# Kernel optimization log

Measured on AMD Instinct MI355X. Metric: run time of the kernel, lower is better.

## Reference

```python
import jax, jax.numpy as jnp
import numpy as np

N_NODES = 50000
N_EDGES = 800000
F_IN = 11
HID = 128
N_ACT = 6


def _gcn_conv(x, W, b, src, dst, n):
    # PyG GCNConv: x' = D^{-1/2}(A+I)D^{-1/2} (x W) + b, with self-loops.
    h = x @ W  # [N, H]
    ones = jnp.ones(src.shape[0], dtype=h.dtype)
    deg = jax.ops.segment_sum(ones, dst, num_segments=n) + 1.0  # +1 self-loop
    dinv = jax.lax.rsqrt(deg)
    enorm = dinv[src] * dinv[dst]  # [E]
    msg = h[src] * enorm[:, None]  # gather + scale
    agg = jax.ops.segment_sum(msg, dst, num_segments=n)
    agg = agg + h * (dinv * dinv)[:, None]  # self-loop contribution (norm = 1/deg)
    return agg + b


def _mlp2(x, W1, b1, W2, b2):
    return jax.nn.relu(x @ W1 + b1) @ W2 + b2


def setup_inputs() -> dict:
    key = jax.random.key(0)
    ks = jax.random.split(key, 16)
    def g(k, shape, scale):
        return jax.random.normal(k, shape, dtype=jnp.float32) * scale
    x = g(ks[0], (N_NODES, F_IN), 1.0)
    edge_index = jax.random.randint(ks[1], (2, N_EDGES), 0, N_NODES, dtype=jnp.int64)
    return {
        "x": x,
        "edge_index": edge_index,
        "W1": g(ks[2], (F_IN, HID), 1.0 / np.sqrt(F_IN)),
        "b1": jnp.zeros((HID,), jnp.float32),
        "W2": g(ks[3], (HID, HID), 1.0 / np.sqrt(HID)),
        "b2": jnp.zeros((HID,), jnp.float32),
        "W3": g(ks[4], (HID, HID), 1.0 / np.sqrt(HID)),
        "b3": jnp.zeros((HID,), jnp.float32),
        "Wv1": g(ks[5], (HID, HID), 1.0 / np.sqrt(HID)),
        "bv1": jnp.zeros((HID,), jnp.float32),
        "Wv2": g(ks[6], (HID, 1), 1.0 / np.sqrt(HID)),
        "bv2": jnp.zeros((1,), jnp.float32),
        "Wa1": g(ks[7], (HID, HID), 1.0 / np.sqrt(HID)),
        "ba1": jnp.zeros((HID,), jnp.float32),
        "Wa2": g(ks[8], (HID, N_ACT), 1.0 / np.sqrt(HID)),
        "ba2": jnp.zeros((N_ACT,), jnp.float32),
    }


def reference(x, edge_index, W1, b1, W2, b2, W3, b3,
              Wv1, bv1, Wv2, bv2, Wa1, ba1, Wa2, ba2):
    src, dst = edge_index[0], edge_index[1]
    n = x.shape[0]
    h = jax.nn.relu(_gcn_conv(x, W1, b1, src, dst, n))
    h = jax.nn.relu(_gcn_conv(h, W2, b2, src, dst, n))
    h = jax.nn.relu(_gcn_conv(h, W3, b3, src, dst, n))
    # global_mean_pool with batch = zeros -> single-graph mean over nodes
    g = jnp.mean(h, axis=0, keepdims=True)  # [1, HID]
    value = _mlp2(g, Wv1, bv1, Wv2, bv2)          # [1, 1]
    advantage = _mlp2(g, Wa1, ba1, Wa2, ba2)      # [1, N_ACT]
    q = value + (advantage - jnp.mean(advantage, axis=-1, keepdims=True))
    return q
```

## Files before the change

kernel.cpp:

```cpp
#include <hip/hip_runtime.h>

#define HID 128
#define F_IN 11
#define FP 16
#define N_ACT 6
#define EPB 2048
#define LMAX 6144
#define CAP 8192

typedef __bf16 bf16;
typedef __bf16 v8bf __attribute__((ext_vector_type(8)));
typedef float f32x4 __attribute__((ext_vector_type(4)));
typedef float v2f __attribute__((ext_vector_type(2)));

__device__ inline float lo16(unsigned u) { return __uint_as_float(u << 16); }
__device__ inline float hi16(unsigned u) { return __uint_as_float(u & 0xffff0000u); }
__device__ inline unsigned pk2(float a, float b) {
  union { bf16 h; unsigned short u; } x, y;
  x.h = (bf16)a; y.h = (bf16)b;
  return ((unsigned)y.u << 16) | x.u;
}
__device__ inline v2f fp8_dec_lo(unsigned v) {
  return __builtin_amdgcn_cvt_pk_f32_fp8(v, false);
}
__device__ inline v2f fp8_dec_hi(unsigned v) {
  return __builtin_amdgcn_cvt_pk_f32_fp8(v, true);
}
__device__ inline unsigned fp8_enc2_lo(float a, float b, unsigned old) {
  return __builtin_amdgcn_cvt_pk_fp8_f32(a, b, old, false);
}
__device__ inline unsigned fp8_enc2_hi(float a, float b, unsigned old) {
  return __builtin_amdgcn_cvt_pk_fp8_f32(a, b, old, true);
}
__device__ inline unsigned char fp8_enc1(float v) {
  return (unsigned char)(__builtin_amdgcn_cvt_pk_fp8_f32(v, v, 0u, false) & 0xffu);
}


__global__ __launch_bounds__(256) void k_init(int* __restrict__ gcur,
                                              float* __restrict__ gsum, int nbkt) {
  int t = threadIdx.x;
  if (t < nbkt) gcur[t] = t * CAP;
  if (t < HID) gsum[t] = 0.f;
}

__global__ __launch_bounds__(256) void k_part(const int* __restrict__ esrc,
                                              const int* __restrict__ edst,
                                              int* __restrict__ gcur,
                                              unsigned* __restrict__ ebuf,
                                              const float* __restrict__ W2,
                                              const float* __restrict__ W3,
                                              bf16* __restrict__ WT2,
                                              bf16* __restrict__ WT3,
                                              int E, int nbkt) {
  __shared__ int hist[256], lofs[256], lcur[256], gbase[256];
  __shared__ unsigned sbuf[EPB];
  int t = threadIdx.x;
  hist[t] = 0;
  if (blockIdx.x < 64) {
    int i = blockIdx.x * 256 + t;
    int nn = i >> 7, k = i & 127;
    WT2[i] = (bf16)W2[k * 128 + nn];
    WT3[i] = (bf16)W3[k * 128 + nn];
  }
  __syncthreads();
  int start = blockIdx.x * EPB, end = min(E, start + EPB);
  unsigned u[8];
#pragma unroll
  for (int i = 0; i < 8; ++i) {
    int e = start + t + i * 256;
    if (e < end) {
      int s = esrc[e], d = edst[e];
      u[i] = ((unsigned)d << 16) | (unsigned)s;
      atomicAdd(&hist[d >> 8], 1);
    }
  }
  __syncthreads();
  int h = hist[t];
  lofs[t] = h;
  __syncthreads();
  for (int off = 1; off < 256; off <<= 1) {
    int x = (t >= off) ? lofs[t - off] : 0;
    __syncthreads();
    lofs[t] += x;
    __syncthreads();
  }
  lcur[t] = lofs[t] - h;
  if (t < nbkt && h) gbase[t] = atomicAdd(&gcur[t], h);
  __syncthreads();
#pragma unroll
  for (int i = 0; i < 8; ++i) {
    int e = start + t + i * 256;
    if (e < end) {
      int b = (int)(u[i] >> 24);
      int p = atomicAdd(&lcur[b], 1);
      sbuf[p] = u[i];
    }
  }
  __syncthreads();
  int m = end - start;
  for (int i = t; i < m; i += 256) {
    unsigned v = sbuf[i];
    int b = (int)(v >> 24);
    int excl = lofs[b] - hist[b];
    ebuf[gbase[b] + (i - excl)] = v;
  }
}

__global__ __launch_bounds__(1024) void k_local(const unsigned* __restrict__ ebuf,
                                                const int* __restrict__ gcur,
                                                int2* __restrict__ rbe,
                                                float* __restrict__ dinv,
                                                unsigned short* __restrict__ cs,
                                                const float* __restrict__ x,
                                                bf16* __restrict__ xs, int n) {
  __shared__ int hist[256], lofs[256], cur[256];
  __shared__ float dsh[256];
  __shared__ unsigned sb[LMAX];
  int b = blockIdx.x, t = threadIdx.x;
  int rb = b * CAP, re = gcur[b];
  int m = re - rb;
  int nbase = b << 8;
  bool fit = (m <= LMAX);
  if (t < 256) hist[t] = 0;
  __syncthreads();
  if (fit) {
    for (int i = t; i < m; i += 1024) {
      unsigned u = ebuf[rb + i];
      sb[i] = u;
      atomicAdd(&hist[(int)(u >> 16) - nbase], 1);
    }
  } else {
    for (int i = t; i < m; i += 1024)
      atomicAdd(&hist[(int)(ebuf[rb + i] >> 16) - nbase], 1);
  }
  __syncthreads();
  int h = 0;
  if (t < 256) { h = hist[t]; lofs[t] = h; }
  __syncthreads();
  for (int off = 1; off < 256; off <<= 1) {
    int v = (t < 256 && t >= off) ? lofs[t - off] : 0;
    __syncthreads();
    if (t < 256) lofs[t] += v;
    __syncthreads();
  }
  if (t < 256) {
    int excl = lofs[t] - h;
    cur[t] = rb + excl;
    float dv = rsqrtf((float)h + 1.0f);
    dsh[t] = dv;
    int g = nbase + t;
    if (g < n) {
      rbe[g] = make_int2(rb + excl, rb + lofs[t]);
      dinv[g] = dv;
    }
  }
  __syncthreads();
  if (fit) {
    for (int i = t; i < m; i += 1024) {
      unsigned u = sb[i];
      int p = atomicAdd(&cur[(int)(u >> 16) - nbase], 1);
      cs[p] = (unsigned short)(u & 0xffffu);
    }
  } else {
    for (int i = t; i < m; i += 1024) {
      unsigned u = ebuf[rb + i];
      int p = atomicAdd(&cur[(int)(u >> 16) - nbase], 1);
      cs[p] = (unsigned short)(u & 0xffffu);
    }
  }
  for (int i = t; i < 256 * FP; i += 1024) {
    int node = nbase + (i >> 4), c = i & 15;
    if (node < n)
      xs[(size_t)node * FP + c] =
          (bf16)((c < F_IN) ? x[(size_t)node * F_IN + c] * dsh[i >> 4] : 0.f);
  }
}


__global__ __launch_bounds__(256) void k_layer1(const bf16* __restrict__ xs,
                                                const float* __restrict__ dinv,
                                                const int2* __restrict__ rbe,
                                                const unsigned short* __restrict__ cs,
                                                const float* __restrict__ W1,
                                                const float* __restrict__ b1,
                                                unsigned* __restrict__ H8, int n) {
  __shared__ float Ws[F_IN * HID];
  __shared__ float A1s[64][17];
  int tid = threadIdx.x;
  int n0 = blockIdx.x * 64;
  for (int i = tid; i < F_IN * HID; i += 256) Ws[i] = W1[i];
  int wave = tid >> 6, lane = tid & 63;
  int g8 = lane >> 3, c = lane & 7;
  const unsigned* xs2 = (const unsigned*)xs;
#pragma unroll
  for (int r = 0; r < 2; ++r) {
    int row = wave * 16 + r * 8 + g8;
    int node = n0 + row;
    unsigned sv = 0;
    int j = 0, jend = 0;
    float dd = 0.f;
    if (node < n) {
      sv = xs2[(size_t)node * 8 + c];
      int2 be = rbe[node];
      j = be.x; jend = be.y;
      dd = dinv[node];
    }
    float ax = lo16(sv), ay = hi16(sv);
    for (; j < jend; j += 4) {
#pragma unroll
      for (int k = 0; k < 4; ++k) {
        int jj = j + k;
        bool ok = jj < jend;
        int sidx = cs[ok ? jj : jend - 1];
        unsigned v = xs2[(size_t)sidx * 8 + c];
        float mm = ok ? 1.f : 0.f;
        ax = fmaf(lo16(v), mm, ax);
        ay = fmaf(hi16(v), mm, ay);
      }
    }
    A1s[row][c * 2] = ax * dd;
    A1s[row][c * 2 + 1] = ay * dd;
  }
  __syncthreads();
  int tc = tid & 15, tr = tid >> 4;
  float bb[8];
#pragma unroll
  for (int j = 0; j < 8; ++j) bb[j] = b1[tc * 8 + j];
#pragma unroll
  for (int i = 0; i < 4; ++i) {
    int row = tr * 4 + i;
    int node = n0 + row;
    if (node >= n) continue;
    float acc[8];
#pragma unroll
    for (int j = 0; j < 8; ++j) acc[j] = 0.f;
#pragma unroll
    for (int k = 0; k < F_IN; ++k) {
      float xk = A1s[row][k];
      const float* wr = &Ws[k * HID + tc * 8];
#pragma unroll
      for (int j = 0; j < 8; ++j) acc[j] = fmaf(xk, wr[j], acc[j]);
    }
    float dd = dinv[node];
    float o[8];
#pragma unroll
    for (int j = 0; j < 8; ++j) o[j] = fmaxf(acc[j] + bb[j], 0.f) * dd;
    unsigned w0 = 0, w1 = 0;
    w0 = fp8_enc2_lo(o[0], o[1], w0);
    w0 = fp8_enc2_hi(o[2], o[3], w0);
    w1 = fp8_enc2_lo(o[4], o[5], w1);
    w1 = fp8_enc2_hi(o[6], o[7], w1);
    ((uint2*)H8)[(size_t)node * 16 + tc] = make_uint2(w0, w1);
  }
}


template <bool FINAL>
__global__ __launch_bounds__(512) void k_layer(const unsigned* __restrict__ tab,
                                               const float* __restrict__ dinv,
                                               const int2* __restrict__ rbe,
                                               const unsigned short* __restrict__ cs,
                                               const bf16* __restrict__ WT,
                                               const float* __restrict__ b,
                                               unsigned char* __restrict__ H8,
                                               float* __restrict__ gsum, int n) {
  __shared__ bf16 Asm[64 * 128];
  __shared__ float colacc[128];
  int tid = threadIdx.x;
  int n0 = blockIdx.x * 64;
  if (FINAL && tid < 128) colacc[tid] = 0.f;
  int wave = tid >> 6, lane = tid & 63;
  int sub = lane >> 5;
  int c = lane & 31;
#pragma unroll
  for (int r = 0; r < 4; ++r) {
    int row = wave * 8 + r * 2 + sub;
    int node = n0 + row;
    float a0 = 0.f, a1 = 0.f, a2 = 0.f, a3 = 0.f, dd = 0.f;
    int j = 0, jend = 0;
    if (node < n) {
      unsigned sv = tab[(size_t)node * 32 + c];
      v2f lo = fp8_dec_lo(sv), hi = fp8_dec_hi(sv);
      a0 = lo.x; a1 = lo.y; a2 = hi.x; a3 = hi.y;
      int2 be = rbe[node];
      j = be.x; jend = be.y;
      dd = dinv[node];
    }
    for (; j < jend; j += 8) {
#pragma unroll
      for (int k = 0; k < 8; ++k) {
        int jj = j + k;
        bool ok = jj < jend;
        int sidx = cs[ok ? jj : jend - 1];
        unsigned v = tab[(size_t)sidx * 32 + c];
        float mm = ok ? 1.f : 0.f;
        v2f lo = fp8_dec_lo(v), hi = fp8_dec_hi(v);
        a0 = fmaf(lo.x, mm, a0);
        a1 = fmaf(lo.y, mm, a1);
        a2 = fmaf(hi.x, mm, a2);
        a3 = fmaf(hi.y, mm, a3);
      }
    }
    int kc = c >> 1, half = c & 1;
    uint2 w = make_uint2(pk2(a0 * dd, a1 * dd), pk2(a2 * dd, a3 * dd));
    *(uint2*)((char*)Asm + row * 256 + ((kc ^ (row & 7)) << 4) + (half << 3)) = w;
  }
  __syncthreads();
  int l15 = lane & 15, g = lane >> 4;
  int rg = (wave & 3) * 16;
  int cg = (wave >> 2) * 64;
  f32x4 acc[4];
#pragma unroll
  for (int f = 0; f < 4; ++f) acc[f] = (f32x4){0.f, 0.f, 0.f, 0.f};
  int arow = rg + l15;
#pragma unroll
  for (int kk = 0; kk < 4; ++kk) {
    int kc = kk * 4 + g;
    v8bf a = *(const v8bf*)((const char*)Asm + arow * 256 + ((kc ^ (arow & 7)) << 4));
#pragma unroll
    for (int f = 0; f < 4; ++f) {
      int nrow = cg + f * 16 + l15;
      v8bf bfr = *(const v8bf*)(WT + (size_t)nrow * 128 + kc * 8);
      acc[f] = __builtin_amdgcn_mfma_f32_16x16x32_bf16(a, bfr, acc[f], 0, 0, 0);
    }
  }
  int nodebase = n0 + rg + g * 4;
  if (FINAL) {
#pragma unroll
    for (int f = 0; f < 4; ++f) {
      int col = cg + f * 16 + l15;
      float bias = b[col];
      float sf = 0.f;
#pragma unroll
      for (int j = 0; j < 4; ++j) {
        int node = nodebase + j;
        if (node < n) sf += fmaxf(acc[f][j] + bias, 0.f);
      }
      atomicAdd(&colacc[col], sf);
    }
    __syncthreads();
    if (tid < 128) atomicAdd(&gsum[tid], colacc[tid]);
  } else {
    float dv[4];
#pragma unroll
    for (int j = 0; j < 4; ++j)
      dv[j] = (nodebase + j < n) ? dinv[nodebase + j] : 1.f;
#pragma unroll
    for (int f = 0; f < 4; ++f) {
      int col = cg + f * 16 + l15;
      float bias = b[col];
#pragma unroll
      for (int j = 0; j < 4; ++j) {
        int node = nodebase + j;
        if (node < n) {
          float v = fmaxf(acc[f][j] + bias, 0.f) * dv[j];
          H8[(size_t)node * 128 + col] = fp8_enc1(v);
        }
      }
    }
  }
}


__global__ __launch_bounds__(128) void k_head(const float* __restrict__ gsum,
    const float* __restrict__ Wv1, const float* __restrict__ bv1,
    const float* __restrict__ Wv2, const float* __restrict__ bv2,
    const float* __restrict__ Wa1, const float* __restrict__ ba1,
    const float* __restrict__ Wa2, const float* __restrict__ ba2,
    float* __restrict__ out, int n) {
  __shared__ float gs[HID], ha[HID], red[2], advs[N_ACT], vsh;
  int t = threadIdx.x;
  gs[t] = gsum[t] * (1.0f / (float)n);
  __syncthreads();
  float av = bv1[t], aa = ba1[t];
  for (int k = 0; k < HID; ++k) {
    float gk = gs[k];
    av = fmaf(gk, Wv1[k * HID + t], av);
    aa = fmaf(gk, Wa1[k * HID + t], aa);
  }
  float hv = fmaxf(av, 0.f);
  ha[t] = fmaxf(aa, 0.f);
  float pv = hv * Wv2[t];
#pragma unroll
  for (int o = 32; o > 0; o >>= 1) pv += __shfl_down(pv, o);
  if ((t & 63) == 0) red[t >> 6] = pv;
  __syncthreads();
  if (t == 0) vsh = red[0] + red[1] + bv2[0];
  if (t < N_ACT) {
    float adv = ba2[t];
    for (int j = 0; j < HID; ++j) adv = fmaf(ha[j], Wa2[j * N_ACT + t], adv);
    advs[t] = adv;
  }
  __syncthreads();
  if (t < N_ACT) {
    float m = 0.f;
#pragma unroll
    for (int a = 0; a < N_ACT; ++a) m += advs[a];
    m *= (1.0f / N_ACT);
    out[t] = vsh + advs[t] - m;
  }
}


extern "C" void kernel_launch(void* const* d_in, const int* in_sizes, int n_in,
                              void* d_out, int out_size, void* d_ws, size_t ws_size,
                              hipStream_t stream) {
  const float* x   = (const float*)d_in[0];
  const int*   ei  = (const int*)d_in[1];
  const float* W1  = (const float*)d_in[2];
  const float* b1  = (const float*)d_in[3];
  const float* W2  = (const float*)d_in[4];
  const float* b2  = (const float*)d_in[5];
  const float* W3  = (const float*)d_in[6];
  const float* b3  = (const float*)d_in[7];
  const float* Wv1 = (const float*)d_in[8];
  const float* bv1 = (const float*)d_in[9];
  const float* Wv2 = (const float*)d_in[10];
  const float* bv2 = (const float*)d_in[11];
  const float* Wa1 = (const float*)d_in[12];
  const float* ba1 = (const float*)d_in[13];
  const float* Wa2 = (const float*)d_in[14];
  const float* ba2 = (const float*)d_in[15];
  float* out = (float*)d_out;

  const int N = in_sizes[0] / F_IN;
  const int E = in_sizes[1] / 2;
  const int* esrc = ei;
  const int* edst = ei + E;
  const int nbkt = (N + 255) >> 8;
  const int gE = (E + EPB - 1) / EPB;

  char* p = (char*)d_ws;
  auto alloc = [&](size_t bytes) {
    void* r = (void*)p;
    p += (bytes + 1023) & ~(size_t)1023;
    return r;
  };
  unsigned* ebuf   = (unsigned*)alloc((size_t)nbkt * CAP * 4);
  int*   gcur      = (int*)alloc((size_t)nbkt * 4);
  int2*  rbe       = (int2*)alloc((size_t)N * 8);
  float* dinv      = (float*)alloc((size_t)N * 4);
  unsigned short* cs = (unsigned short*)alloc((size_t)nbkt * CAP * 2);
  bf16*  xs        = (bf16*)alloc((size_t)N * FP * 2);
  bf16*  WT2       = (bf16*)alloc(128 * 128 * 2);
  bf16*  WT3       = (bf16*)alloc(128 * 128 * 2);
  unsigned* H8a    = (unsigned*)alloc((size_t)N * 128);
  unsigned* H8b    = (unsigned*)alloc((size_t)N * 128);
  float* gsum      = (float*)alloc(HID * 4);

  k_init<<<1, 256, 0, stream>>>(gcur, gsum, nbkt);
  k_part<<<gE, 256, 0, stream>>>(esrc, edst, gcur, ebuf, W2, W3, WT2, WT3, E, nbkt);
  k_local<<<nbkt, 1024, 0, stream>>>(ebuf, gcur, rbe, dinv, cs, x, xs, N);

  k_layer1<<<(N + 63) / 64, 256, 0, stream>>>(xs, dinv, rbe, cs, W1, b1, H8a, N);

  int gL = (N + 63) / 64;
  k_layer<false><<<gL, 512, 0, stream>>>(H8a, dinv, rbe, cs, WT2, b2,
                                         (unsigned char*)H8b, gsum, N);
  k_layer<true><<<gL, 512, 0, stream>>>(H8b, dinv, rbe, cs, WT3, b3,
                                        (unsigned char*)nullptr, gsum, N);

  k_head<<<1, 128, 0, stream>>>(gsum, Wv1, bv1, Wv2, bv2, Wa1, ba1, Wa2, ba2, out, N);
}
```

Baseline: 146.9 us.

## Pad CSR neighbor lists to multiples of 16 with zero-row sentinel, unmask gathers

Each node's neighbor segment in the CSR index array is padded up to a multiple of 16. The padding entries point to a sentinel node n whose feature rows (xs, H8a, H8b) are zeroed in k_init. This removes the per-edge bounds masking from the gather loops. The k_layer gather now loads 16 indices at once with two aligned uint4 loads, issues 16 independent feature loads, and halves the node tile per block from 64 to 32 to launch more blocks. The cost is extra gathers of the cached zero row and more CSR capacity use per bucket, which could overflow CAP on skewed graphs.

```diff
diff --git a/kernel.cpp b/kernel.cpp
--- a/kernel.cpp
+++ b/kernel.cpp
@@ -38,11 +38,17 @@
 
 
 __global__ __launch_bounds__(256) void k_init(int* __restrict__ gcur,
-                                              float* __restrict__ gsum, int nbkt) {
+                                              float* __restrict__ gsum,
+                                              unsigned* __restrict__ xsN,
+                                              unsigned* __restrict__ H8aN,
+                                              unsigned* __restrict__ H8bN, int nbkt) {
   int t = threadIdx.x;
   if (t < nbkt) gcur[t] = t * CAP;
   if (t < HID) gsum[t] = 0.f;
-}
+  if (t < 8) xsN[t] = 0u;
+  if (t < 32) { H8aN[t] = 0u; H8bN[t] = 0u; }
+}
+
 
 __global__ __launch_bounds__(256) void k_part(const int* __restrict__ esrc,
                                               const int* __restrict__ edst,
@@ -114,7 +120,7 @@
                                                 unsigned short* __restrict__ cs,
                                                 const float* __restrict__ x,
                                                 bf16* __restrict__ xs, int n) {
-  __shared__ int hist[256], lofs[256], cur[256];
+  __shared__ int hist[256], lofs[256], cur[256], realh[256];
   __shared__ float dsh[256];
   __shared__ unsigned sb[LMAX];
   int b = blockIdx.x, t = threadIdx.x;
@@ -135,8 +141,13 @@
       atomicAdd(&hist[(int)(ebuf[rb + i] >> 16) - nbase], 1);
   }
   __syncthreads();
-  int h = 0;
-  if (t < 256) { h = hist[t]; lofs[t] = h; }
+  int h = 0, hp = 0;
+  if (t < 256) {
+    h = hist[t];
+    realh[t] = h;
+    hp = (h + 15) & ~15;
+    lofs[t] = hp;
+  }
   __syncthreads();
   for (int off = 1; off < 256; off <<= 1) {
     int v = (t < 256 && t >= off) ? lofs[t - off] : 0;
@@ -145,13 +156,13 @@
     __syncthreads();
   }
   if (t < 256) {
-    int excl = lofs[t] - h;
-    cur[t] = rb + excl;
+    int pexcl = lofs[t] - hp;
+    cur[t] = rb + pexcl;
     float dv = rsqrtf((float)h + 1.0f);
     dsh[t] = dv;
     int g = nbase + t;
     if (g < n) {
-      rbe[g] = make_int2(rb + excl, rb + lofs[t]);
+      rbe[g] = make_int2(rb + pexcl, rb + pexcl + hp);
       dinv[g] = dv;
     }
   }
@@ -168,6 +179,13 @@
       int p = atomicAdd(&cur[(int)(u >> 16) - nbase], 1);
       cs[p] = (unsigned short)(u & 0xffffu);
     }
+  }
+  __syncthreads();
+  if (t < 256) {
+    int hh = realh[t];
+    int hpp = (hh + 15) & ~15;
+    int base = cur[t];
+    for (int i = hh; i < hpp; ++i) cs[base + (i - hh)] = (unsigned short)n;
   }
   for (int i = t; i < 256 * FP; i += 1024) {
     int node = nbase + (i >> 4), c = i & 15;
@@ -210,13 +228,9 @@
     for (; j < jend; j += 4) {
 #pragma unroll
       for (int k = 0; k < 4; ++k) {
-        int jj = j + k;
-        bool ok = jj < jend;
-        int sidx = cs[ok ? jj : jend - 1];
-        unsigned v = xs2[(size_t)sidx * 8 + c];
-        float mm = ok ? 1.f : 0.f;
-        ax = fmaf(lo16(v), mm, ax);
-        ay = fmaf(hi16(v), mm, ay);
+        unsigned v = xs2[(size_t)cs[j + k] * 8 + c];
+        ax += lo16(v);
+        ay += hi16(v);
       }
     }
     A1s[row][c * 2] = ax * dd;
@@ -265,62 +279,70 @@
                                                const float* __restrict__ b,
                                                unsigned char* __restrict__ H8,
                                                float* __restrict__ gsum, int n) {
-  __shared__ bf16 Asm[64 * 128];
+  __shared__ bf16 Asm[32 * 128];
   __shared__ float colacc[128];
   int tid = threadIdx.x;
-  int n0 = blockIdx.x * 64;
+  int n0 = blockIdx.x * 32;
   if (FINAL && tid < 128) colacc[tid] = 0.f;
   int wave = tid >> 6, lane = tid & 63;
   int sub = lane >> 5;
   int c = lane & 31;
 #pragma unroll
-  for (int r = 0; r < 4; ++r) {
-    int row = wave * 8 + r * 2 + sub;
+  for (int r = 0; r < 2; ++r) {
+    int row = wave * 4 + r * 2 + sub;
     int node = n0 + row;
-    float a0 = 0.f, a1 = 0.f, a2 = 0.f, a3 = 0.f, dd = 0.f;
+    v2f acc01 = (v2f){0.f, 0.f}, acc23 = (v2f){0.f, 0.f};
+    float dd = 0.f;
     int j = 0, jend = 0;
     if (node < n) {
       unsigned sv = tab[(size_t)node * 32 + c];
-      v2f lo = fp8_dec_lo(sv), hi = fp8_dec_hi(sv);
-      a0 = lo.x; a1 = lo.y; a2 = hi.x; a3 = hi.y;
+      acc01 = fp8_dec_lo(sv);
+      acc23 = fp8_dec_hi(sv);
       int2 be = rbe[node];
       j = be.x; jend = be.y;
       dd = dinv[node];
     }
-    for (; j < jend; j += 8) {
-#pragma unroll
-      for (int k = 0; k < 8; ++k) {
-        int jj = j + k;
-        bool ok = jj < jend;
-        int sidx = cs[ok ? jj : jend - 1];
-        unsigned v = tab[(size_t)sidx * 32 + c];
-        float mm = ok ? 1.f : 0.f;
-        v2f lo = fp8_dec_lo(v), hi = fp8_dec_hi(v);
-        a0 = fmaf(lo.x, mm, a0);
-        a1 = fmaf(lo.y, mm, a1);
-        a2 = fmaf(hi.x, mm, a2);
-        a3 = fmaf(hi.y, mm, a3);
+    for (; j < jend; j += 16) {
+      uint4 cv0 = *(const uint4*)(cs + j);
+      uint4 cv1 = *(const uint4*)(cs + j + 8);
+      unsigned sx[16];
+      sx[0] = cv0.x & 0xffffu;  sx[1] = cv0.x >> 16;
+      sx[2] = cv0.y & 0xffffu;  sx[3] = cv0.y >> 16;
+      sx[4] = cv0.z & 0xffffu;  sx[5] = cv0.z >> 16;
+      sx[6] = cv0.w & 0xffffu;  sx[7] = cv0.w >> 16;
+      sx[8] = cv1.x & 0xffffu;  sx[9] = cv1.x >> 16;
+      sx[10] = cv1.y & 0xffffu; sx[11] = cv1.y >> 16;
+      sx[12] = cv1.z & 0xffffu; sx[13] = cv1.z >> 16;
+      sx[14] = cv1.w & 0xffffu; sx[15] = cv1.w >> 16;
+      unsigned vv[16];
+#pragma unroll
+      for (int k = 0; k < 16; ++k) vv[k] = tab[(size_t)sx[k] * 32 + c];
+#pragma unroll
+      for (int k = 0; k < 16; ++k) {
+        acc01 += fp8_dec_lo(vv[k]);
+        acc23 += fp8_dec_hi(vv[k]);
       }
     }
     int kc = c >> 1, half = c & 1;
-    uint2 w = make_uint2(pk2(a0 * dd, a1 * dd), pk2(a2 * dd, a3 * dd));
+    uint2 w = make_uint2(pk2(acc01.x * dd, acc01.y * dd),
+                         pk2(acc23.x * dd, acc23.y * dd));
     *(uint2*)((char*)Asm + row * 256 + ((kc ^ (row & 7)) << 4) + (half << 3)) = w;
   }
   __syncthreads();
   int l15 = lane & 15, g = lane >> 4;
-  int rg = (wave & 3) * 16;
-  int cg = (wave >> 2) * 64;
-  f32x4 acc[4];
-#pragma unroll
-  for (int f = 0; f < 4; ++f) acc[f] = (f32x4){0.f, 0.f, 0.f, 0.f};
+  int rg = (wave & 1) * 16;
+  int cbase = (wave >> 1) * 32;
+  f32x4 acc[2];
+#pragma unroll
+  for (int f = 0; f < 2; ++f) acc[f] = (f32x4){0.f, 0.f, 0.f, 0.f};
   int arow = rg + l15;
 #pragma unroll
   for (int kk = 0; kk < 4; ++kk) {
     int kc = kk * 4 + g;
     v8bf a = *(const v8bf*)((const char*)Asm + arow * 256 + ((kc ^ (arow & 7)) << 4));
 #pragma unroll
-    for (int f = 0; f < 4; ++f) {
-      int nrow = cg + f * 16 + l15;
+    for (int f = 0; f < 2; ++f) {
+      int nrow = cbase + f * 16 + l15;
       v8bf bfr = *(const v8bf*)(WT + (size_t)nrow * 128 + kc * 8);
       acc[f] = __builtin_amdgcn_mfma_f32_16x16x32_bf16(a, bfr, acc[f], 0, 0, 0);
     }
@@ -328,8 +350,8 @@
   int nodebase = n0 + rg + g * 4;
   if (FINAL) {
 #pragma unroll
-    for (int f = 0; f < 4; ++f) {
-      int col = cg + f * 16 + l15;
+    for (int f = 0; f < 2; ++f) {
+      int col = cbase + f * 16 + l15;
       float bias = b[col];
       float sf = 0.f;
 #pragma unroll
@@ -347,8 +369,8 @@
     for (int j = 0; j < 4; ++j)
       dv[j] = (nodebase + j < n) ? dinv[nodebase + j] : 1.f;
 #pragma unroll
-    for (int f = 0; f < 4; ++f) {
-      int col = cg + f * 16 + l15;
+    for (int f = 0; f < 2; ++f) {
+      int col = cbase + f * 16 + l15;
       float bias = b[col];
 #pragma unroll
       for (int j = 0; j < 4; ++j) {
@@ -442,20 +464,21 @@
   int2*  rbe       = (int2*)alloc((size_t)N * 8);
   float* dinv      = (float*)alloc((size_t)N * 4);
   unsigned short* cs = (unsigned short*)alloc((size_t)nbkt * CAP * 2);
-  bf16*  xs        = (bf16*)alloc((size_t)N * FP * 2);
+  bf16*  xs        = (bf16*)alloc((size_t)(N + 1) * FP * 2);
   bf16*  WT2       = (bf16*)alloc(128 * 128 * 2);
   bf16*  WT3       = (bf16*)alloc(128 * 128 * 2);
-  unsigned* H8a    = (unsigned*)alloc((size_t)N * 128);
-  unsigned* H8b    = (unsigned*)alloc((size_t)N * 128);
+  unsigned* H8a    = (unsigned*)alloc((size_t)(N + 1) * 128);
+  unsigned* H8b    = (unsigned*)alloc((size_t)(N + 1) * 128);
   float* gsum      = (float*)alloc(HID * 4);
 
-  k_init<<<1, 256, 0, stream>>>(gcur, gsum, nbkt);
+  k_init<<<1, 256, 0, stream>>>(gcur, gsum, (unsigned*)(xs + (size_t)N * FP),
+                                H8a + (size_t)N * 32, H8b + (size_t)N * 32, nbkt);
   k_part<<<gE, 256, 0, stream>>>(esrc, edst, gcur, ebuf, W2, W3, WT2, WT3, E, nbkt);
   k_local<<<nbkt, 1024, 0, stream>>>(ebuf, gcur, rbe, dinv, cs, x, xs, N);
 
   k_layer1<<<(N + 63) / 64, 256, 0, stream>>>(xs, dinv, rbe, cs, W1, b1, H8a, N);
 
-  int gL = (N + 63) / 64;
+  int gL = (N + 31) / 32;
   k_layer<false><<<gL, 512, 0, stream>>>(H8a, dinv, rbe, cs, WT2, b2,
                                          (unsigned char*)H8b, gsum, N);
   k_layer<true><<<gL, 512, 0, stream>>>(H8b, dinv, rbe, cs, WT3, b3,
```

Result: no change. 145.9 us (median of 2 runs) (-0.7%).
